# Kernel optimization log

Measured on AMD Instinct MI355X. Metric: run time of the kernel, lower is better.

## Reference

```python
import jax, jax.numpy as jnp
import numpy as np

B, N, F = 2, 2048, 1024
H = 16
DH = F // H  # features per head = 64
SCALE = 1.0 / np.sqrt(DH)


def setup_inputs() -> dict:
    key = jax.random.key(0)
    ks = jax.random.split(key, 11)
    s = 0.02
    return {
        "q": jax.random.normal(ks[0], (B, N, F), dtype=jnp.float32),
        "k": jax.random.normal(ks[1], (B, N, F), dtype=jnp.float32),
        "v": jax.random.normal(ks[2], (B, N, F), dtype=jnp.float32),
        "Wq": jax.random.normal(ks[3], (F, F), dtype=jnp.float32) * s,
        "bq": jnp.zeros((F,), dtype=jnp.float32),
        "Wk": jax.random.normal(ks[4], (F, F), dtype=jnp.float32) * s,
        "bk": jnp.zeros((F,), dtype=jnp.float32),
        "Wv": jax.random.normal(ks[5], (F, F), dtype=jnp.float32) * s,
        "bv": jnp.zeros((F,), dtype=jnp.float32),
        "Wo": jax.random.normal(ks[6], (F, F), dtype=jnp.float32) * s,
        "bo": jnp.zeros((F,), dtype=jnp.float32),
    }


def reference(q, k, v, Wq, bq, Wk, bk, Wv, bv, Wo, bo):
    b = q.shape[0]
    # projections, split into heads: [B, H, N, DH]
    qh = (q @ Wq + bq).reshape(b, -1, H, DH).transpose(0, 2, 1, 3)
    kh = (k @ Wk + bk).reshape(b, -1, H, DH).transpose(0, 2, 1, 3)
    vh = (v @ Wv + bv).reshape(b, -1, H, DH).transpose(0, 2, 1, 3)
    # scaled dot-product attention
    attn = jnp.einsum("bhqd,bhkd->bhqk", qh * SCALE, kh)
    attn = jax.nn.softmax(attn, axis=-1)
    out = jnp.einsum("bhqk,bhkd->bhqd", attn, vh)
    # merge heads: [B, Nq, F]
    out = out.transpose(0, 2, 1, 3).reshape(b, -1, H * DH)
    return out @ Wo + bo
```

## Files before the change

kernel.cpp:

```cpp
#include <hip/hip_runtime.h>
#include <hip/hip_bf16.h>

typedef float f32x4  __attribute__((ext_vector_type(4)));
typedef float f32x16 __attribute__((ext_vector_type(16)));
typedef short s16x8  __attribute__((ext_vector_type(8)));
typedef unsigned int u32;
typedef unsigned short u16;
typedef u16 u16x4 __attribute__((ext_vector_type(4)));
typedef u32 u32x4 __attribute__((ext_vector_type(4)));

#define DEVI static __device__ __forceinline__

constexpr int BB   = 2;
constexpr int SEQ  = 2048;
constexpr int FD   = 1024;
constexpr int NH   = 16;
constexpr int DHD  = 64;

DEVI u16 f2bf(float x){
  __hip_bfloat16 h = __float2bfloat16(x);
  return __builtin_bit_cast(u16, h);
}
DEVI float bf2f(u16 u){
  return __bfloat162float(__builtin_bit_cast(__hip_bfloat16, u));
}
DEVI u32 pack2(float a, float b){
  return (u32)f2bf(a) | ((u32)f2bf(b) << 16);
}

DEVI void mfma_bf16(f32x4& acc, s16x8 a, s16x8 b){
  asm("v_mfma_f32_16x16x32_bf16 %0, %1, %2, %0" : "+v"(acc) : "v"(a), "v"(b));
}
DEVI void mfma32(f32x16& acc, s16x8 a, s16x8 b){
  asm("v_mfma_f32_32x32x16_bf16 %0, %1, %2, %0" : "+v"(acc) : "v"(a), "v"(b));
}
DEVI void plswap(u32& a, u32& b){
  asm("v_permlane32_swap_b32 %0, %1" : "+v"(a), "+v"(b));
}

#define AS1C(p) ((const __attribute__((address_space(1))) void*)(p))
#define AS3(p)  ((__attribute__((address_space(3))) void*)(p))

__global__ __launch_bounds__(256) void wprep_all(
    const float* __restrict__ W0, const float* __restrict__ W1,
    const float* __restrict__ W2, const float* __restrict__ W3,
    u16* __restrict__ T0, u16* __restrict__ T1,
    u16* __restrict__ T2, u16* __restrict__ T3)
{
  const int z = blockIdx.z;
  const float* W = z==0?W0 : z==1?W1 : z==2?W2 : W3;
  u16* Th       = z==0?T0 : z==1?T1 : z==2?T2 : T3;

  __shared__ float tile[64][65];
  const int kb = blockIdx.x * 64, nb = blockIdx.y * 64;
  const int t  = threadIdx.x;
  const int r  = t >> 2, c0 = (t & 3) * 16;

  const float* src = W + (size_t)(kb + r) * FD + nb + c0;
  #pragma unroll
  for (int i = 0; i < 16; i += 4){
    float4 v = *reinterpret_cast<const float4*>(src + i);
    tile[r][c0+i+0] = v.x; tile[r][c0+i+1] = v.y;
    tile[r][c0+i+2] = v.z; tile[r][c0+i+3] = v.w;
  }
  __syncthreads();

  s16x8 hA, hB;
  #pragma unroll
  for (int i = 0; i < 8; i++){
    hA[i] = (short)f2bf(tile[c0 + i][r]);
    hB[i] = (short)f2bf(tile[c0 + 8 + i][r]);
  }
  const size_t o = (size_t)(nb + r) * FD + kb + c0;
  *reinterpret_cast<s16x8*>(Th + o)     = hA;
  *reinterpret_cast<s16x8*>(Th + o + 8) = hB;
}

__global__ __launch_bounds__(256, 3) void qkv_gemm(
    const float* __restrict__ qp, const float* __restrict__ kp, const float* __restrict__ vp,
    const u16* __restrict__ Wq, const u16* __restrict__ Wk, const u16* __restrict__ Wv,
    const float* __restrict__ bq, const float* __restrict__ bk, const float* __restrict__ bv,
    u16* __restrict__ Q2, u16* __restrict__ K2, u16* __restrict__ Vt2)
{
  __shared__ float sA[2][128*32];
  __shared__ u16   sW[2][128*32];

  const int bid  = blockIdx.x;
  const int xcd  = bid & 7, idx = bid >> 3;
  const int strip = xcd * 12 + (idx >> 3);
  const int nb   = idx & 7;
  const int z    = strip >> 5, my = strip & 31;

  const float* Ap   = z==0?qp : z==1?kp : vp;
  const u16*  Wh    = z==0?Wq : z==1?Wk : Wv;
  const float* bias = z==0?bq : z==1?bk : bv;
  u16* outp         = z==0?Q2 : z==1?K2 : Vt2;
  const float oscale = (z==0) ? 0.125f : 1.0f;
  const bool  tr     = (z==2);

  const int t    = threadIdx.x;
  const int nb0  = nb * 128, mb0 = my * 128;
  const int lane = t & 63, w = t >> 6;
  const int r16  = lane & 15, g = lane >> 4;
  const int wm   = (w >> 1) * 64, wn = (w & 1) * 64;

  const int aRow = lane >> 3, aChunk = (lane & 7) ^ aRow;
  const int wRow = lane >> 2, wChunk = (lane & 3) ^ (wRow & 3);

  auto stage = [&](int buf, int kb){
    #pragma unroll
    for (int i = 0; i < 4; i++){
      const int row = i*32 + w*8 + aRow;
      const float* ag = Ap + (size_t)(mb0 + row) * FD + kb + aChunk*4;
      __builtin_amdgcn_global_load_lds(AS1C(ag), AS3(&sA[buf][(i*32 + w*8)*32]), 16, 0, 0);
    }
    #pragma unroll
    for (int i = 0; i < 2; i++){
      const int row = i*64 + w*16 + wRow;
      const u16* wg = Wh + (size_t)(nb0 + row) * FD + kb + wChunk*8;
      __builtin_amdgcn_global_load_lds(AS1C(wg), AS3(&sW[buf][(i*64 + w*16)*32]), 16, 0, 0);
    }
  };
  auto ldsA = [&](const float* base, int row, int gg) -> s16x8 {
    const char* p = reinterpret_cast<const char*>(base);
    const int roff = row << 7, sw = (row & 7) << 4;
    f32x4 lo = *reinterpret_cast<const f32x4*>(p + (roff + ((gg*32)      ^ sw)));
    f32x4 hi = *reinterpret_cast<const f32x4*>(p + (roff + ((gg*32 + 16) ^ sw)));
    s16x8 r;
    #pragma unroll
    for (int j = 0; j < 4; j++){
      r[j]   = (short)f2bf(lo[j]);
      r[4+j] = (short)f2bf(hi[j]);
    }
    return r;
  };
  auto ldsW = [&](const u16* base, int row, int gg) -> s16x8 {
    const char* p = reinterpret_cast<const char*>(base);
    const int off = (row << 6) + ((gg*16) ^ ((row & 3) << 4));
    return *reinterpret_cast<const s16x8*>(p + off);
  };

  f32x4 acc[4][4] = {};

  stage(0, 0);
  __syncthreads();

  for (int it = 0; it < FD/32; it++){
    const int buf = it & 1;
    if (it + 1 < FD/32) stage(buf ^ 1, (it + 1) * 32);

    s16x8 a[4], bh[4];
    #pragma unroll
    for (int i = 0; i < 4; i++)
      a[i]  = ldsA(sA[buf], wm + i*16 + r16, g);
    #pragma unroll
    for (int j = 0; j < 4; j++)
      bh[j] = ldsW(sW[buf], wn + j*16 + r16, g);

    __builtin_amdgcn_s_setprio(1);
    #pragma unroll
    for (int i = 0; i < 4; i++)
      #pragma unroll
      for (int j = 0; j < 4; j++)
        mfma_bf16(acc[i][j], a[i], bh[j]);
    __builtin_amdgcn_s_setprio(0);

    __syncthreads();
  }

  #pragma unroll
  for (int i = 0; i < 4; i++){
    #pragma unroll
    for (int j = 0; j < 4; j++){
      const int ccol = nb0 + wn + j*16 + r16;
      const float bv = bias[ccol];
      #pragma unroll
      for (int r = 0; r < 4; r++){
        const int m = mb0 + wm + i*16 + g*4 + r;
        const float v = (acc[i][j][r] + bv) * oscale;
        const int b = m >> 11, n = m & (SEQ - 1);
        const int h = ccol >> 6, d = ccol & 63;
        const size_t o = tr ? ((size_t)(b*NH + h)*DHD + d)*SEQ + n
                            : ((size_t)(b*NH + h)*SEQ + n)*DHD + d;
        outp[o] = f2bf(v);
      }
    }
  }
}

__global__ __launch_bounds__(256, 3) void ogemm_k(
    const u16* __restrict__ Ap, const u16* __restrict__ Wh,
    const float* __restrict__ bias, float* __restrict__ outp)
{
  __shared__ u16 sA[2][64*32];
  __shared__ u16 sW[2][128*32];

  const int bid  = blockIdx.x;
  const int xcd  = bid & 7, idx = bid >> 3;
  const int my   = xcd * 8 + (idx >> 3);
  const int nb   = idx & 7;

  const int t    = threadIdx.x;
  const int nb0  = nb * 128, mb0 = my * 64;
  const int lane = t & 63, w = t >> 6;
  const int r16  = lane & 15, g = lane >> 4;
  const int wm   = (w >> 1) * 32, wn = (w & 1) * 64;

  const int wRow = lane >> 2, wChunk = (lane & 3) ^ (wRow & 3);

  auto stage = [&](int buf, int kb){
    {
      const int row = w*16 + wRow;
      const u16* ag = Ap + (size_t)(mb0 + row) * FD + kb + wChunk*8;
      __builtin_amdgcn_global_load_lds(AS1C(ag), AS3(&sA[buf][(w*16)*32]), 16, 0, 0);
    }
    #pragma unroll
    for (int i = 0; i < 2; i++){
      const int row = i*64 + w*16 + wRow;
      const u16* wg = Wh + (size_t)(nb0 + row) * FD + kb + wChunk*8;
      __builtin_amdgcn_global_load_lds(AS1C(wg), AS3(&sW[buf][(i*64 + w*16)*32]), 16, 0, 0);
    }
  };
  auto ldsW = [&](const u16* base, int row, int gg) -> s16x8 {
    const char* p = reinterpret_cast<const char*>(base);
    const int off = (row << 6) + ((gg*16) ^ ((row & 3) << 4));
    return *reinterpret_cast<const s16x8*>(p + off);
  };

  f32x4 acc[2][4] = {};

  stage(0, 0);
  __syncthreads();

  for (int it = 0; it < FD/32; it++){
    const int buf = it & 1;
    if (it + 1 < FD/32) stage(buf ^ 1, (it + 1) * 32);

    s16x8 a[2], bh[4];
    #pragma unroll
    for (int i = 0; i < 2; i++)
      a[i]  = ldsW(sA[buf], wm + i*16 + r16, g);
    #pragma unroll
    for (int j = 0; j < 4; j++)
      bh[j] = ldsW(sW[buf], wn + j*16 + r16, g);

    __builtin_amdgcn_s_setprio(1);
    #pragma unroll
    for (int i = 0; i < 2; i++)
      #pragma unroll
      for (int j = 0; j < 4; j++)
        mfma_bf16(acc[i][j], a[i], bh[j]);
    __builtin_amdgcn_s_setprio(0);

    __syncthreads();
  }

  #pragma unroll
  for (int i = 0; i < 2; i++){
    #pragma unroll
    for (int j = 0; j < 4; j++){
      const int ccol = nb0 + wn + j*16 + r16;
      const float bv = bias[ccol];
      #pragma unroll
      for (int r = 0; r < 4; r++){
        const int m = mb0 + wm + i*16 + g*4 + r;
        outp[(size_t)m * FD + ccol] = acc[i][j][r] + bv;
      }
    }
  }
}

__global__ __launch_bounds__(512, 4) void attn_k(
    const u16* __restrict__ Q2, const u16* __restrict__ K2, const u16* __restrict__ Vt2,
    u16* __restrict__ AOh)
{
  __shared__ u16 smem[2][2][2][64*64];

  const int bid = blockIdx.x + 16 * blockIdx.y;
  const int qt  = bid >> 5;
  const int bh  = (bid & 7) * 4 + ((bid >> 3) & 3);

  const int t = threadIdx.x, w = t >> 6, lane = t & 63;
  const int grp = w >> 2, gw = w & 3;
  const int l31 = lane & 31, hi = lane >> 5;

  const u16* Kb = K2  + (size_t)bh * SEQ * DHD;
  const u16* Vb = Vt2 + (size_t)bh * DHD * SEQ;

  const int srow8  = lane >> 3;
  const int schunk = ((lane & 7) ^ srow8) * 8;

  const int qrow = qt*128 + gw*32 + l31;
  const u16* Qrow = Q2 + ((size_t)bh * SEQ + qrow) * DHD;
  s16x8 qf[4];
  #pragma unroll
  for (int dk = 0; dk < 4; dk++)
    qf[dk] = *reinterpret_cast<const s16x8*>(Qrow + dk*16 + hi*8);

  f32x16 ot0 = {}, ot1 = {};
  float mrun = -1e30f, lrun = 0.f;

  auto stage_tile = [&](int buf, int kt){
    #pragma unroll
    for (int i = 0; i < 2; i++){
      const int row = gw*16 + i*8 + srow8;
      const u16* kg = Kb + (size_t)(kt*64 + row) * DHD + schunk;
      const u16* vg = Vb + (size_t)row * SEQ + kt*64 + schunk;
      __builtin_amdgcn_global_load_lds(AS1C(kg), AS3(&smem[0][grp][buf][(gw*16 + i*8)*64]), 16, 0, 0);
      __builtin_amdgcn_global_load_lds(AS1C(vg), AS3(&smem[1][grp][buf][(gw*16 + i*8)*64]), 16, 0, 0);
    }
  };
  auto lds16 = [](const u16* base, int row, int colbyte) -> s16x8 {
    int off = (row << 7) + colbyte;
    off ^= (row & 7) << 4;
    return *reinterpret_cast<const s16x8*>(reinterpret_cast<const char*>(base) + off);
  };

  constexpr int NIT = SEQ / 64 / 2;
  stage_tile(0, grp);
  __syncthreads();

  for (int i = 0; i < NIT; i++){
    const int buf = i & 1;
    if (i + 1 < NIT) stage_tile(buf ^ 1, 2*(i+1) + grp);
    const u16* sK = &smem[0][grp][buf][0];
    const u16* sV = &smem[1][grp][buf][0];

    f32x16 st0 = {}, st1 = {};
    __builtin_amdgcn_s_setprio(1);
    #pragma unroll
    for (int dk = 0; dk < 4; dk++){
      s16x8 kf0 = lds16(sK, l31,      dk*32 + hi*16);
      s16x8 kf1 = lds16(sK, 32 + l31, dk*32 + hi*16);
      mfma32(st0, kf0, qf[dk]);
      mfma32(st1, kf1, qf[dk]);
    }
    __builtin_amdgcn_s_setprio(0);

    float mx[8];
    #pragma unroll
    for (int r = 0; r < 8; r++)
      mx[r] = fmaxf(fmaxf(st0[r], st0[r+8]), fmaxf(st1[r], st1[r+8]));
    float pmax = fmaxf(fmaxf(fmaxf(mx[0],mx[1]), fmaxf(mx[2],mx[3])),
                       fmaxf(fmaxf(mx[4],mx[5]), fmaxf(mx[6],mx[7])));
    pmax = fmaxf(pmax, __shfl_xor(pmax, 32, 64));

    if (!__all(pmax <= mrun + 8.f)){
      float mnew = fmaxf(mrun, pmax);
      float alp = __expf(mrun - mnew);
      mrun = mnew;
      lrun *= alp;
      #pragma unroll
      for (int r = 0; r < 16; r++){ ot0[r] *= alp; ot1[r] *= alp; }
    }

    #pragma unroll
    for (int r = 0; r < 16; r++){
      st0[r] = __expf(st0[r] - mrun);
      st1[r] = __expf(st1[r] - mrun);
    }
    float s8[8];
    #pragma unroll
    for (int r = 0; r < 8; r++)
      s8[r] = (st0[r] + st0[r+8]) + (st1[r] + st1[r+8]);
    float psum = ((s8[0]+s8[1])+(s8[2]+s8[3])) + ((s8[4]+s8[5])+(s8[6]+s8[7]));
    psum += __shfl_xor(psum, 32, 64);
    lrun += psum;

    u32 pw[16];
    #pragma unroll
    for (int g2 = 0; g2 < 4; g2++){
      pw[g2*2+0]   = pack2(st0[g2*4+0], st0[g2*4+1]);
      pw[g2*2+1]   = pack2(st0[g2*4+2], st0[g2*4+3]);
      pw[8+g2*2+0] = pack2(st1[g2*4+0], st1[g2*4+1]);
      pw[8+g2*2+1] = pack2(st1[g2*4+2], st1[g2*4+3]);
    }
    s16x8 pb[4];
    #pragma unroll
    for (int ks = 0; ks < 4; ks++){
      const int e = (ks>>1)*8 + (ks&1)*4;
      u32 w0 = pw[e+0], w1 = pw[e+1], w2 = pw[e+2], w3 = pw[e+3];
      plswap(w0, w2);
      plswap(w1, w3);
      u32x4 wv = { w0, w1, w2, w3 };
      pb[ks] = __builtin_bit_cast(s16x8, wv);
    }

    __builtin_amdgcn_s_setprio(1);
    #pragma unroll
    for (int ks = 0; ks < 4; ks++){
      s16x8 vf0 = lds16(sV, l31,      ks*32 + hi*16);
      s16x8 vf1 = lds16(sV, 32 + l31, ks*32 + hi*16);
      mfma32(ot0, vf0, pb[ks]);
      mfma32(ot1, vf1, pb[ks]);
    }
    __builtin_amdgcn_s_setprio(0);

    __syncthreads();
  }

  float* sO = reinterpret_cast<float*>(&smem[0][0][0][0]);
  float* sM = reinterpret_cast<float*>(&smem[0][0][0][0]) + 128*68;
  const int ql = gw*32 + l31;

  if (grp == 1){
    #pragma unroll
    for (int r4 = 0; r4 < 4; r4++){
      const int d0 = r4*8 + hi*4;
      #pragma unroll
      for (int j = 0; j < 4; j++){
        sO[ql*68 + d0 + j]      = ot0[r4*4+j];
        sO[ql*68 + 32 + d0 + j] = ot1[r4*4+j];
      }
    }
    if (hi == 0){ sM[ql*2+0] = mrun; sM[ql*2+1] = lrun; }
  }
  __syncthreads();
  if (grp == 0){
    const float m1 = sM[ql*2+0], l1 = sM[ql*2+1];
    const float M  = fmaxf(mrun, m1);
    const float w0 = __expf(mrun - M), w1e = __expf(m1 - M);
    const float inv = 1.0f / (lrun*w0 + l1*w1e);

    const int b = bh >> 4, h = bh & 15;
    u16* orow = AOh + ((size_t)b*SEQ + qrow) * FD + h*64;
    #pragma unroll
    for (int r4 = 0; r4 < 4; r4++){
      const int d0 = r4*8 + hi*4;
      u16x4 v0, v1;
      #pragma unroll
      for (int j = 0; j < 4; j++){
        v0[j] = f2bf((ot0[r4*4+j]*w0 + sO[ql*68 + d0 + j]*w1e) * inv);
        v1[j] = f2bf((ot1[r4*4+j]*w0 + sO[ql*68 + 32 + d0 + j]*w1e) * inv);
      }
      *reinterpret_cast<u16x4*>(orow + d0)      = v0;
      *reinterpret_cast<u16x4*>(orow + 32 + d0) = v1;
    }
  }
}

extern "C" void kernel_launch(void* const* d_in, const int* in_sizes, int n_in,
                              void* d_out, int out_size, void* d_ws, size_t ws_size,
                              hipStream_t stream)
{
  const float* q  = (const float*)d_in[0];
  const float* k  = (const float*)d_in[1];
  const float* v  = (const float*)d_in[2];
  const float* Wq = (const float*)d_in[3];
  const float* bq = (const float*)d_in[4];
  const float* Wk = (const float*)d_in[5];
  const float* bk = (const float*)d_in[6];
  const float* Wv = (const float*)d_in[7];
  const float* bv = (const float*)d_in[8];
  const float* Wo = (const float*)d_in[9];
  const float* bo = (const float*)d_in[10];
  float* out = (float*)d_out;
  (void)in_sizes; (void)n_in; (void)out_size; (void)ws_size;

  char* ws = (char*)d_ws;
  size_t off = 0;
  auto alloc = [&](size_t bytes) -> char* {
    char* p = ws + off;
    off += (bytes + 255) & ~(size_t)255;
    return p;
  };
  const size_t WB = (size_t)FD * FD * sizeof(u16);
  u16* WqTh = (u16*)alloc(WB);
  u16* WkTh = (u16*)alloc(WB);
  u16* WvTh = (u16*)alloc(WB);
  u16* WoTh = (u16*)alloc(WB);
  const size_t QB = (size_t)BB * NH * SEQ * DHD * sizeof(u16);
  u16* Q2  = (u16*)alloc(QB);
  u16* K2  = (u16*)alloc(QB);
  u16* Vt2 = (u16*)alloc(QB);
  const size_t AB = (size_t)BB * SEQ * FD * sizeof(u16);
  u16* AOh = (u16*)alloc(AB);

  wprep_all<<<dim3(16,16,4), 256, 0, stream>>>(Wq, Wk, Wv, Wo, WqTh, WkTh, WvTh, WoTh);

  qkv_gemm<<<dim3(768), 256, 0, stream>>>(q, k, v, WqTh, WkTh, WvTh,
                                          bq, bk, bv, Q2, K2, Vt2);

  attn_k<<<dim3(16,32), 512, 0, stream>>>(Q2, K2, Vt2, AOh);

  ogemm_k<<<dim3(512), 256, 0, stream>>>(AOh, WoTh, bo, out);
}
```

Baseline: 138.5 us.

## Pre-convert activations to bf16 and restructure GEMM pipelines with explicit waitcnts

Adds a separate kernel that converts the q/k/v fp32 activations to bf16 up front, so the QKV GEMM stages bf16 tiles into LDS directly instead of loading fp32 and converting per fragment. Both GEMMs now prefetch two stages ahead, using explicit vmcnt/lgkmcnt waits and raw barriers in place of __syncthreads, and use a new LDS swizzle. The extra conversion pass costs additional global traffic for writing and re-reading the bf16 activations. It also halves the LDS footprint of the A tile.

After: 142.2 us. +2.7%, slower.

```diff
diff --git a/kernel.cpp b/kernel.cpp
--- a/kernel.cpp
+++ b/kernel.cpp
@@ -16,6 +16,7 @@
 constexpr int FD   = 1024;
 constexpr int NH   = 16;
 constexpr int DHD  = 64;
+constexpr int MROWS = BB * SEQ;
 
 DEVI u16 f2bf(float x){
   __hip_bfloat16 h = __float2bfloat16(x);
@@ -40,6 +41,27 @@
 
 #define AS1C(p) ((const __attribute__((address_space(1))) void*)(p))
 #define AS3(p)  ((__attribute__((address_space(3))) void*)(p))
+
+#define VMCNT(n)  asm volatile("s_waitcnt vmcnt(" #n ")" ::: "memory")
+#define LGKMCNT0  asm volatile("s_waitcnt lgkmcnt(0)" ::: "memory")
+DEVI void barrier(){ __builtin_amdgcn_s_barrier(); __builtin_amdgcn_sched_barrier(0); }
+
+__global__ __launch_bounds__(256) void tobf16(
+    const float* __restrict__ q, const float* __restrict__ k,
+    const float* __restrict__ v, u16* __restrict__ o)
+{
+  const size_t n1 = (size_t)MROWS * FD;
+  const size_t i  = ((size_t)blockIdx.x * 256 + threadIdx.x) * 8;
+  const float* src = (i < n1) ? q + i : (i < 2*n1 ? k + (i - n1) : v + (i - 2*n1));
+  float4 v0 = *reinterpret_cast<const float4*>(src);
+  float4 v1 = *reinterpret_cast<const float4*>(src + 4);
+  s16x8 r;
+  r[0]=(short)f2bf(v0.x); r[1]=(short)f2bf(v0.y);
+  r[2]=(short)f2bf(v0.z); r[3]=(short)f2bf(v0.w);
+  r[4]=(short)f2bf(v1.x); r[5]=(short)f2bf(v1.y);
+  r[6]=(short)f2bf(v1.z); r[7]=(short)f2bf(v1.w);
+  *reinterpret_cast<s16x8*>(o + i) = r;
+}
 
 __global__ __launch_bounds__(256) void wprep_all(
     const float* __restrict__ W0, const float* __restrict__ W1,
@@ -76,14 +98,19 @@
   *reinterpret_cast<s16x8*>(Th + o + 8) = hB;
 }
 
+DEVI s16x8 ldsT(const u16* base, int row, int g){
+  const char* p = reinterpret_cast<const char*>(base);
+  return *reinterpret_cast<const s16x8*>(p + (row << 6) + ((g ^ ((row >> 1) & 3)) << 4));
+}
+
 __global__ __launch_bounds__(256, 3) void qkv_gemm(
-    const float* __restrict__ qp, const float* __restrict__ kp, const float* __restrict__ vp,
+    const u16* __restrict__ Abase,
     const u16* __restrict__ Wq, const u16* __restrict__ Wk, const u16* __restrict__ Wv,
     const float* __restrict__ bq, const float* __restrict__ bk, const float* __restrict__ bv,
     u16* __restrict__ Q2, u16* __restrict__ K2, u16* __restrict__ Vt2)
 {
-  __shared__ float sA[2][128*32];
-  __shared__ u16   sW[2][128*32];
+  __shared__ u16 sA[2][128*32];
+  __shared__ u16 sW[2][128*32];
 
   const int bid  = blockIdx.x;
   const int xcd  = bid & 7, idx = bid >> 3;
@@ -91,7 +118,7 @@
   const int nb   = idx & 7;
   const int z    = strip >> 5, my = strip & 31;
 
-  const float* Ap   = z==0?qp : z==1?kp : vp;
+  const u16* Ap     = Abase + (size_t)z * MROWS * FD;
   const u16*  Wh    = z==0?Wq : z==1?Wk : Wv;
   const float* bias = z==0?bq : z==1?bk : bv;
   u16* outp         = z==0?Q2 : z==1?K2 : Vt2;
@@ -104,58 +131,42 @@
   const int r16  = lane & 15, g = lane >> 4;
   const int wm   = (w >> 1) * 64, wn = (w & 1) * 64;
 
-  const int aRow = lane >> 3, aChunk = (lane & 7) ^ aRow;
-  const int wRow = lane >> 2, wChunk = (lane & 3) ^ (wRow & 3);
+  const int sRow   = lane >> 2;
+  const int sChunk = (lane & 3);
 
   auto stage = [&](int buf, int kb){
     #pragma unroll
-    for (int i = 0; i < 4; i++){
-      const int row = i*32 + w*8 + aRow;
-      const float* ag = Ap + (size_t)(mb0 + row) * FD + kb + aChunk*4;
-      __builtin_amdgcn_global_load_lds(AS1C(ag), AS3(&sA[buf][(i*32 + w*8)*32]), 16, 0, 0);
-    }
-    #pragma unroll
     for (int i = 0; i < 2; i++){
-      const int row = i*64 + w*16 + wRow;
-      const u16* wg = Wh + (size_t)(nb0 + row) * FD + kb + wChunk*8;
-      __builtin_amdgcn_global_load_lds(AS1C(wg), AS3(&sW[buf][(i*64 + w*16)*32]), 16, 0, 0);
+      const int row = w*32 + i*16 + sRow;
+      const int gch = sChunk ^ ((row >> 1) & 3);
+      const u16* ag = Ap + (size_t)(mb0 + row) * FD + kb + gch*8;
+      const u16* wg = Wh + (size_t)(nb0 + row) * FD + kb + gch*8;
+      __builtin_amdgcn_global_load_lds(AS1C(ag), AS3(&sA[buf][(w*32 + i*16)*32]), 16, 0, 0);
+      __builtin_amdgcn_global_load_lds(AS1C(wg), AS3(&sW[buf][(w*32 + i*16)*32]), 16, 0, 0);
     }
   };
-  auto ldsA = [&](const float* base, int row, int gg) -> s16x8 {
-    const char* p = reinterpret_cast<const char*>(base);
-    const int roff = row << 7, sw = (row & 7) << 4;
-    f32x4 lo = *reinterpret_cast<const f32x4*>(p + (roff + ((gg*32)      ^ sw)));
-    f32x4 hi = *reinterpret_cast<const f32x4*>(p + (roff + ((gg*32 + 16) ^ sw)));
-    s16x8 r;
-    #pragma unroll
-    for (int j = 0; j < 4; j++){
-      r[j]   = (short)f2bf(lo[j]);
-      r[4+j] = (short)f2bf(hi[j]);
-    }
-    return r;
-  };
-  auto ldsW = [&](const u16* base, int row, int gg) -> s16x8 {
-    const char* p = reinterpret_cast<const char*>(base);
-    const int off = (row << 6) + ((gg*16) ^ ((row & 3) << 4));
-    return *reinterpret_cast<const s16x8*>(p + off);
-  };
 
   f32x4 acc[4][4] = {};
 
   stage(0, 0);
-  __syncthreads();
+  stage(1, 32);
+  VMCNT(4);
+  barrier();
 
   for (int it = 0; it < FD/32; it++){
     const int buf = it & 1;
-    if (it + 1 < FD/32) stage(buf ^ 1, (it + 1) * 32);
 
     s16x8 a[4], bh[4];
     #pragma unroll
     for (int i = 0; i < 4; i++)
-      a[i]  = ldsA(sA[buf], wm + i*16 + r16, g);
+      a[i]  = ldsT(sA[buf], wm + i*16 + r16, g);
     #pragma unroll
     for (int j = 0; j < 4; j++)
-      bh[j] = ldsW(sW[buf], wn + j*16 + r16, g);
+      bh[j] = ldsT(sW[buf], wn + j*16 + r16, g);
+    LGKMCNT0;
+    barrier();
+
+    if (it + 2 < FD/32) stage(buf, (it + 2) * 32);
 
     __builtin_amdgcn_s_setprio(1);
     #pragma unroll
@@ -165,7 +176,9 @@
         mfma_bf16(acc[i][j], a[i], bh[j]);
     __builtin_amdgcn_s_setprio(0);
 
-    __syncthreads();
+    if (it + 2 < FD/32) { VMCNT(4); }
+    else                { VMCNT(0); }
+    barrier();
   }
 
   #pragma unroll
@@ -206,43 +219,46 @@
   const int r16  = lane & 15, g = lane >> 4;
   const int wm   = (w >> 1) * 32, wn = (w & 1) * 64;
 
-  const int wRow = lane >> 2, wChunk = (lane & 3) ^ (wRow & 3);
+  const int sRow   = lane >> 2;
+  const int sChunk = (lane & 3);
 
   auto stage = [&](int buf, int kb){
     {
-      const int row = w*16 + wRow;
-      const u16* ag = Ap + (size_t)(mb0 + row) * FD + kb + wChunk*8;
+      const int row = w*16 + sRow;
+      const int gch = sChunk ^ ((row >> 1) & 3);
+      const u16* ag = Ap + (size_t)(mb0 + row) * FD + kb + gch*8;
       __builtin_amdgcn_global_load_lds(AS1C(ag), AS3(&sA[buf][(w*16)*32]), 16, 0, 0);
     }
     #pragma unroll
     for (int i = 0; i < 2; i++){
-      const int row = i*64 + w*16 + wRow;
-      const u16* wg = Wh + (size_t)(nb0 + row) * FD + kb + wChunk*8;
-      __builtin_amdgcn_global_load_lds(AS1C(wg), AS3(&sW[buf][(i*64 + w*16)*32]), 16, 0, 0);
+      const int row = w*32 + i*16 + sRow;
+      const int gch = sChunk ^ ((row >> 1) & 3);
+      const u16* wg = Wh + (size_t)(nb0 + row) * FD + kb + gch*8;
+      __builtin_amdgcn_global_load_lds(AS1C(wg), AS3(&sW[buf][(w*32 + i*16)*32]), 16, 0, 0);
     }
   };
-  auto ldsW = [&](const u16* base, int row, int gg) -> s16x8 {
-    const char* p = reinterpret_cast<const char*>(base);
-    const int off = (row << 6) + ((gg*16) ^ ((row & 3) << 4));
-    return *reinterpret_cast<const s16x8*>(p + off);
-  };
 
   f32x4 acc[2][4] = {};
 
   stage(0, 0);
-  __syncthreads();
+  stage(1, 32);
+  VMCNT(3);
+  barrier();
 
   for (int it = 0; it < FD/32; it++){
     const int buf = it & 1;
-    if (it + 1 < FD/32) stage(buf ^ 1, (it + 1) * 32);
 
     s16x8 a[2], bh[4];
     #pragma unroll
     for (int i = 0; i < 2; i++)
-      a[i]  = ldsW(sA[buf], wm + i*16 + r16, g);
+      a[i]  = ldsT(sA[buf], wm + i*16 + r16, g);
     #pragma unroll
     for (int j = 0; j < 4; j++)
-      bh[j] = ldsW(sW[buf], wn + j*16 + r16, g);
+      bh[j] = ldsT(sW[buf], wn + j*16 + r16, g);
+    LGKMCNT0;
+    barrier();
+
+    if (it + 2 < FD/32) stage(buf, (it + 2) * 32);
 
     __builtin_amdgcn_s_setprio(1);
     #pragma unroll
@@ -252,7 +268,9 @@
         mfma_bf16(acc[i][j], a[i], bh[j]);
     __builtin_amdgcn_s_setprio(0);
 
-    __syncthreads();
+    if (it + 2 < FD/32) { VMCNT(3); }
+    else                { VMCNT(0); }
+    barrier();
   }
 
   #pragma unroll
@@ -475,10 +493,13 @@
   u16* Vt2 = (u16*)alloc(QB);
   const size_t AB = (size_t)BB * SEQ * FD * sizeof(u16);
   u16* AOh = (u16*)alloc(AB);
+  u16* Abf = (u16*)alloc(3 * AB);
+
+  tobf16<<<dim3(3 * MROWS * FD / (256*8)), 256, 0, stream>>>(q, k, v, Abf);
 
   wprep_all<<<dim3(16,16,4), 256, 0, stream>>>(Wq, Wk, Wv, Wo, WqTh, WkTh, WvTh, WoTh);
 
-  qkv_gemm<<<dim3(768), 256, 0, stream>>>(q, k, v, WqTh, WkTh, WvTh,
+  qkv_gemm<<<dim3(768), 256, 0, stream>>>(Abf, WqTh, WkTh, WvTh,
                                           bq, bk, bv, Q2, K2, Vt2);
 
   attn_k<<<dim3(16,32), 512, 0, stream>>>(Q2, K2, Vt2, AOh);
```
